# Performance work log

Hardware: AMD Instinct MI355X
Metric: run time of the kernel (lower is better)

The kernel has to match this reference:

```python
import jax, jax.numpy as jnp
import numpy as np

N_NODES = 100000
N_EDGES = 3200000
F_IN = 256
H = 256
L = 256
BN_EPS = 1e-5


def gcn_conv(x, src, dst, deg_inv_sqrt, W, b):
    # x: [N, Fin]; src/dst: [E+N] (self-loops appended); returns [N, Fout]
    h = x @ W  # dense transform first (Fout may be < Fin)
    norm = deg_inv_sqrt[src] * deg_inv_sqrt[dst]  # [E+N]
    msg = h[src] * norm[:, None]                  # gather
    out = jax.ops.segment_sum(msg, dst, num_segments=N_NODES)  # scatter-add
    return out + b


def batch_norm(x, gamma, beta):
    # BatchNorm1d in training mode: per-feature mean/var over the node dim
    mean = jnp.mean(x, axis=0)
    var = jnp.var(x, axis=0)
    return (x - mean) * jax.lax.rsqrt(var + BN_EPS) * gamma + beta


def setup_inputs() -> dict:
    key = jax.random.key(0)
    ks = jax.random.split(key, 8)
    x = jax.random.normal(ks[0], (N_NODES, F_IN), dtype=jnp.float32)
    edge_index = jax.random.randint(ks[1], (2, N_EDGES), 0, N_NODES, dtype=jnp.int64)
    # glorot-ish init for weights
    W1 = jax.random.normal(ks[2], (F_IN, H), dtype=jnp.float32) * (1.0 / np.sqrt(F_IN))
    b1 = jnp.zeros((H,), dtype=jnp.float32)
    W_mu = jax.random.normal(ks[3], (H, L), dtype=jnp.float32) * (1.0 / np.sqrt(H))
    b_mu = jnp.zeros((L,), dtype=jnp.float32)
    W_ls = jax.random.normal(ks[4], (H, L), dtype=jnp.float32) * (1.0 / np.sqrt(H))
    b_ls = jnp.zeros((L,), dtype=jnp.float32)
    gamma = jnp.ones((H,), dtype=jnp.float32)
    beta = jnp.zeros((H,), dtype=jnp.float32)
    return {"x": x, "edge_index": edge_index, "W1": W1, "b1": b1,
            "W_mu": W_mu, "b_mu": b_mu, "W_ls": W_ls, "b_ls": b_ls,
            "gamma": gamma, "beta": beta}


def reference(x, edge_index, W1, b1, W_mu, b_mu, W_ls, b_ls, gamma, beta):
    # Add self-loops once (shared across the three GCNConv layers)
    loop = jnp.arange(N_NODES, dtype=edge_index.dtype)
    src = jnp.concatenate([edge_index[0], loop])
    dst = jnp.concatenate([edge_index[1], loop])
    deg = jax.ops.segment_sum(jnp.ones_like(dst, dtype=jnp.float32), dst,
                              num_segments=N_NODES)
    deg_inv_sqrt = jnp.where(deg > 0, jax.lax.rsqrt(jnp.maximum(deg, 1.0)), 0.0)

    h = gcn_conv(x, src, dst, deg_inv_sqrt, W1, b1)
    h = jax.nn.relu(batch_norm(h, gamma, beta))
    mu = gcn_conv(h, src, dst, deg_inv_sqrt, W_mu, b_mu)
    logstd = gcn_conv(h, src, dst, deg_inv_sqrt, W_ls, b_ls)
    return (mu, logstd)
```

## Files before the change

### kernel.cpp

```cpp
#include <hip/hip_runtime.h>
#include <hip/hip_bf16.h>

#define FEAT 256
#define NPB 512
#define NPB_SHIFT 9
#define MAXBINS 256
#define CAP 20480
#define BIN_CHUNK 8192

typedef __attribute__((ext_vector_type(8))) short bf16x8;
typedef __attribute__((ext_vector_type(8))) ushort u16x8;
typedef __attribute__((ext_vector_type(4))) float f32x4;

__device__ __forceinline__ float bf2f(ushort h) {
    union { unsigned u; float f; } v; v.u = ((unsigned)h) << 16; return v.f;
}
__device__ __forceinline__ ushort f2bf(float f) {
    union { float f; unsigned u; } v; v.f = f;
    unsigned u = v.u;
    return (ushort)((u + 0x7FFFu + ((u >> 16) & 1u)) >> 16);
}


__global__ __launch_bounds__(256) void k_bin(const int* __restrict__ ei, int E, int N,
                                             int* __restrict__ bincur,
                                             int2* __restrict__ binbuf, int nbins) {
    __shared__ int hist[MAXBINS];
    __shared__ int base[MAXBINS];
    int t = threadIdx.x;
    int T = E + N;
    int start = blockIdx.x * BIN_CHUNK;
    int end = min(start + BIN_CHUNK, T);
    for (int b = t; b < nbins; b += 256) hist[b] = 0;
    __syncthreads();
    for (int idx = start + t; idx < end; idx += 256) {
        int d = (idx < E) ? ei[E + idx] : idx - E;
        atomicAdd(&hist[d >> NPB_SHIFT], 1);
    }
    __syncthreads();
    for (int b = t; b < nbins; b += 256) {
        int c = hist[b];
        base[b] = c ? (b * CAP + atomicAdd(&bincur[b], c)) : 0;
        hist[b] = 0;
    }
    __syncthreads();
    for (int idx = start + t; idx < end; idx += 256) {
        int s, d;
        if (idx < E) { s = ei[idx]; d = ei[E + idx]; }
        else         { s = idx - E; d = idx - E; }
        int b = d >> NPB_SHIFT;
        int local = atomicAdd(&hist[b], 1);
        binbuf[base[b] + local] = make_int2(s, d);
    }
}


__global__ __launch_bounds__(512) void k_scanb(const int* __restrict__ bsum,
                                               int* __restrict__ bpre,
                                               int* __restrict__ offs_n, int nb) {
    __shared__ int s[512];
    int t = threadIdx.x;
    int v = (t < nb) ? bsum[t] : 0;
    s[t] = v;
    __syncthreads();
    for (int d = 1; d < 512; d <<= 1) {
        int x = (t >= d) ? s[t - d] : 0;
        __syncthreads();
        s[t] += x;
        __syncthreads();
    }
    if (t < nb) bpre[t] = s[t] - v;
    if (t == nb - 1) offs_n[0] = s[t];
}


__global__ __launch_bounds__(512) void k_histoffs(const int2* __restrict__ binbuf,
                                                  const int* __restrict__ bincur,
                                                  const int* __restrict__ bpre,
                                                  int* __restrict__ offs,
                                                  float* __restrict__ dis, int N) {
    __shared__ int h[NPB];
    int b = blockIdx.x;
    int t = threadIdx.x;
    int node0 = b * NPB;
    int nn = min(NPB, N - node0);
    h[t] = 0;
    __syncthreads();
    int cnt = bincur[b];
    int base = b * CAP;
    for (int i = t; i < cnt; i += 512) {
        int d = binbuf[base + i].y;
        atomicAdd(&h[d - node0], 1);
    }
    __syncthreads();
    int v = h[t];
    for (int d = 1; d < 512; d <<= 1) {
        int x = (t >= d) ? h[t - d] : 0;
        __syncthreads();
        h[t] += x;
        __syncthreads();
    }
    if (t < nn) {
        offs[node0 + t] = bpre[b] + h[t] - v;
        dis[node0 + t] = rsqrtf((float)v);
    }
}


__global__ __launch_bounds__(256) void k_csr(const int2* __restrict__ binbuf,
                                             const int* __restrict__ bincur,
                                             const int* __restrict__ offs,
                                             int* __restrict__ csr, int N) {
    __shared__ int soffs[NPB + 1];
    __shared__ int cur[NPB];
    int b = blockIdx.x;
    int node0 = b * NPB;
    int nn = min(NPB, N - node0);
    int t = threadIdx.x;
    for (int i = t; i <= nn; i += 256) soffs[i] = offs[node0 + i];
    for (int i = t; i < nn; i += 256) cur[i] = 0;
    __syncthreads();
    int cnt = bincur[b];
    int base = b * CAP;
    for (int idx = t; idx < cnt; idx += 256) {
        int2 e = binbuf[base + idx];
        int ld = e.y - node0;
        int c = atomicAdd(&cur[ld], 1);
        csr[soffs[ld] + c] = e.x;
    }
}


__global__ __launch_bounds__(256) void k_cvt(const float* __restrict__ x,
                                             ushort* __restrict__ y,
                                             const float* __restrict__ dis, int n4) {
    int i = blockIdx.x * blockDim.x + threadIdx.x;
    int stride = gridDim.x * blockDim.x;
    for (; i < n4; i += stride) {
        float d = dis[i >> 6];
        float4 v = ((const float4*)x)[i];
        ushort4 o;
        o.x = f2bf(v.x * d); o.y = f2bf(v.y * d);
        o.z = f2bf(v.z * d); o.w = f2bf(v.w * d);
        ((ushort4*)y)[i] = o;
    }
}


__global__ void k_wprep(const float* __restrict__ W1, const float* __restrict__ Wmu,
                        const float* __restrict__ Wls, const float* __restrict__ bmu,
                        const float* __restrict__ bls,
                        ushort* __restrict__ Wt1, ushort* __restrict__ Wtc,
                        float* __restrict__ biasc, float* __restrict__ bnacc) {
    int i = blockIdx.x * 256 + threadIdx.x;
    int m = i >> 16;
    int j = i & 65535;
    int n = j >> 8, k = j & 255;
    const float* W = (m == 0) ? W1 : (m == 1) ? Wmu : Wls;
    ushort v = f2bf(W[k * 256 + n]);
    if (m == 0) Wt1[j] = v;
    else if (m == 1) Wtc[j] = v;
    else Wtc[65536 + j] = v;
    if (i < 512) { biasc[i] = (i < 256) ? bmu[i] : bls[i - 256]; bnacc[i] = 0.f; }
}


template <int NCOL, bool BF16OUT>
__global__ __launch_bounds__(256, 4) void k_aggmm(const ushort* __restrict__ tab,
                                                  const int* __restrict__ offs,
                                                  const int* __restrict__ csr,
                                                  const float* __restrict__ dis,
                                                  const ushort* __restrict__ Bt,
                                                  const float* __restrict__ bias,
                                                  float* __restrict__ C0,
                                                  float* __restrict__ C1,
                                                  ushort* __restrict__ Cb,
                                                  float* __restrict__ bnacc,
                                                  int N) {
    __shared__ ushort At[64 * 256];
    __shared__ ushort Bs[64 * 64];
    int t = threadIdx.x;
    int wave = t >> 6;
    int lane = t & 63;
    int half = lane >> 5;
    int l32 = lane & 31;
    int rowbase = blockIdx.x * 64;

    for (int i = 0; i < 16; ++i) {
        int r = wave * 16 + i;
        int node = rowbase + r;
        float acc[8] = {};
        if (node < N) {
            int beg = offs[node], end = offs[node + 1];
            int k = beg;
            for (; k + 16 <= end; k += 16) {
                int s0 = csr[k + half];
                int s1 = csr[k + 2 + half];
                int s2 = csr[k + 4 + half];
                int s3 = csr[k + 6 + half];
                int s4 = csr[k + 8 + half];
                int s5 = csr[k + 10 + half];
                int s6 = csr[k + 12 + half];
                int s7 = csr[k + 14 + half];
                bf16x8 v0 = *(const bf16x8*)(tab + (size_t)s0 * FEAT + l32 * 8);
                bf16x8 v1 = *(const bf16x8*)(tab + (size_t)s1 * FEAT + l32 * 8);
                bf16x8 v2 = *(const bf16x8*)(tab + (size_t)s2 * FEAT + l32 * 8);
                bf16x8 v3 = *(const bf16x8*)(tab + (size_t)s3 * FEAT + l32 * 8);
                bf16x8 v4 = *(const bf16x8*)(tab + (size_t)s4 * FEAT + l32 * 8);
                bf16x8 v5 = *(const bf16x8*)(tab + (size_t)s5 * FEAT + l32 * 8);
                bf16x8 v6 = *(const bf16x8*)(tab + (size_t)s6 * FEAT + l32 * 8);
                bf16x8 v7 = *(const bf16x8*)(tab + (size_t)s7 * FEAT + l32 * 8);
                #pragma unroll
                for (int j = 0; j < 8; ++j) {
                    float t0 = bf2f((ushort)v0[j]) + bf2f((ushort)v1[j]);
                    float t1 = bf2f((ushort)v2[j]) + bf2f((ushort)v3[j]);
                    float t2 = bf2f((ushort)v4[j]) + bf2f((ushort)v5[j]);
                    float t3 = bf2f((ushort)v6[j]) + bf2f((ushort)v7[j]);
                    acc[j] += (t0 + t1) + (t2 + t3);
                }
            }
            for (; k + 2 <= end; k += 2) {
                int s = csr[k + half];
                bf16x8 v = *(const bf16x8*)(tab + (size_t)s * FEAT + l32 * 8);
                #pragma unroll
                for (int j = 0; j < 8; ++j) acc[j] += bf2f((ushort)v[j]);
            }
            if (k < end && half == 0) {
                int s = csr[k];
                bf16x8 v = *(const bf16x8*)(tab + (size_t)s * FEAT + l32 * 8);
                #pragma unroll
                for (int j = 0; j < 8; ++j) acc[j] += bf2f((ushort)v[j]);
            }
        }
        #pragma unroll
        for (int j = 0; j < 8; ++j) acc[j] += __shfl_xor(acc[j], 32, 64);
        if (half == 0) {
            float d = (node < N) ? dis[node] : 0.f;
            u16x8 o;
            #pragma unroll
            for (int j = 0; j < 8; ++j) o[j] = f2bf(acc[j] * d);
            int cs = (l32 & 24) | ((l32 & 7) ^ (r & 7));
            *(u16x8*)(At + r * 256 + cs * 8) = o;
        }
    }
    __syncthreads();

    constexpr int NH = NCOL / 64;
    int wm = wave >> 1, wn = wave & 1;
    int lo = lane & 15, g = lane >> 4;
    for (int nh = 0; nh < NH; ++nh) {
        f32x4 acc2[2][2] = {};
        for (int kt = 0; kt < 4; ++kt) {
            #pragma unroll
            for (int u = 0; u < 2; ++u) {
                int id = t + u * 256;
                int br = id >> 3, bc = id & 7;
                int lc = bc ^ (br & 7);
                bf16x8 bv = *(const bf16x8*)(Bt + (size_t)(nh * 64 + br) * 256 + kt * 64 + lc * 8);
                *(bf16x8*)(Bs + br * 64 + bc * 8) = bv;
            }
            __syncthreads();
            #pragma unroll
            for (int h = 0; h < 2; ++h) {
                bf16x8 af[2], bfr[2];
                #pragma unroll
                for (int m = 0; m < 2; ++m) {
                    int r = wm * 32 + m * 16 + lo;
                    af[m] = *(const bf16x8*)(At + r * 256 + (kt * 8 + ((h * 4 + g) ^ (r & 7))) * 8);
                }
                #pragma unroll
                for (int n = 0; n < 2; ++n) {
                    int rb = wn * 32 + n * 16 + lo;
                    bfr[n] = *(const bf16x8*)(Bs + rb * 64 + ((h * 4 + g) ^ (rb & 7)) * 8);
                }
                #pragma unroll
                for (int m = 0; m < 2; ++m)
                    #pragma unroll
                    for (int n = 0; n < 2; ++n)
                        acc2[m][n] = __builtin_amdgcn_mfma_f32_16x16x32_bf16(
                            af[m], bfr[n], acc2[m][n], 0, 0, 0);
            }
            __syncthreads();
        }
        #pragma unroll
        for (int n = 0; n < 2; ++n) {
            int gc = nh * 64 + wn * 32 + n * 16 + lo;
            float bb = bias[gc];
            float s = 0.f, q = 0.f;
            #pragma unroll
            for (int m = 0; m < 2; ++m) {
                f32x4 v = acc2[m][n];
                #pragma unroll
                for (int r4 = 0; r4 < 4; ++r4) {
                    int grow = rowbase + wm * 32 + m * 16 + g * 4 + r4;
                    if (grow < N) {
                        float val = v[r4] + bb;
                        if (BF16OUT) {
                            Cb[(size_t)grow * 256 + gc] = f2bf(val);
                            s += val; q += val * val;
                        } else {
                            float* Cp = C0; int cc = gc;
                            if (gc >= 256) { Cp = C1; cc = gc - 256; }
                            __builtin_nontemporal_store(val, &Cp[(size_t)grow * 256 + cc]);
                        }
                    }
                }
            }
            if (BF16OUT) {
                s += __shfl_xor(s, 16, 64); s += __shfl_xor(s, 32, 64);
                q += __shfl_xor(q, 16, 64); q += __shfl_xor(q, 32, 64);
                if (g == 0) {
                    atomicAdd(&bnacc[gc], s);
                    atomicAdd(&bnacc[256 + gc], q);
                }
            }
        }
    }
}


__global__ __launch_bounds__(256) void k_bnapply(const ushort* __restrict__ h,
                                                 ushort* __restrict__ o,
                                                 const float* __restrict__ acc,
                                                 const float* __restrict__ gamma,
                                                 const float* __restrict__ beta,
                                                 const float* __restrict__ dis, int Nn) {
    int c4 = (threadIdx.x & 63) * 4;
    int rof = (int)threadIdx.x >> 6;
    float inv = 1.0f / (float)Nn;
    float g[4], b[4];
    #pragma unroll
    for (int j = 0; j < 4; ++j) {
        float mean = acc[c4 + j] * inv;
        float var = acc[FEAT + c4 + j] * inv - mean * mean;
        float rs = rsqrtf(var + 1e-5f);
        g[j] = gamma[c4 + j] * rs;
        b[j] = beta[c4 + j] - mean * g[j];
    }
    for (int r = blockIdx.x * 4 + rof; r < Nn; r += gridDim.x * 4) {
        float d = dis[r];
        ushort4 v = *(const ushort4*)(h + (size_t)r * FEAT + c4);
        float o0 = bf2f(v.x) * g[0] + b[0], o1 = bf2f(v.y) * g[1] + b[1];
        float o2 = bf2f(v.z) * g[2] + b[2], o3 = bf2f(v.w) * g[3] + b[3];
        ushort4 ov;
        ov.x = f2bf((o0 > 0.f ? o0 : 0.f) * d);
        ov.y = f2bf((o1 > 0.f ? o1 : 0.f) * d);
        ov.z = f2bf((o2 > 0.f ? o2 : 0.f) * d);
        ov.w = f2bf((o3 > 0.f ? o3 : 0.f) * d);
        *(ushort4*)(o + (size_t)r * FEAT + c4) = ov;
    }
}


extern "C" void kernel_launch(void* const* d_in, const int* in_sizes, int n_in,
                              void* d_out, int out_size, void* d_ws, size_t ws_size,
                              hipStream_t stream) {
    const float* x     = (const float*)d_in[0];
    const int*   ei    = (const int*)d_in[1];
    const float* W1    = (const float*)d_in[2];
    const float* b1    = (const float*)d_in[3];
    const float* Wmu   = (const float*)d_in[4];
    const float* bmu   = (const float*)d_in[5];
    const float* Wls   = (const float*)d_in[6];
    const float* bls   = (const float*)d_in[7];
    const float* gamma = (const float*)d_in[8];
    const float* beta  = (const float*)d_in[9];

    int N = in_sizes[0] / FEAT;
    int E = in_sizes[1] / 2;
    int nbins = (N + NPB - 1) / NPB;
    int T = E + N;

    float* out = (float*)d_out;
    float* mu  = out;
    float* ls  = out + (size_t)N * FEAT;
    ushort* xtab = (ushort*)mu;
    ushort* H1b  = (ushort*)ls;

    char* p = (char*)d_ws;
    auto alloc = [&](size_t bytes) -> void* {
        void* r = (void*)p;
        p += (bytes + 255) & ~(size_t)255;
        return r;
    };
    ushort* htab  = (ushort*)alloc((size_t)N * FEAT * 2);
    int2*   binbuf= (int2*)  alloc((size_t)nbins * CAP * 8);
    int*    csr   = (int*)   alloc((size_t)T * 4);
    int*    offs  = (int*)   alloc((size_t)(N + 1) * 4);
    float*  dis   = (float*) alloc((size_t)N * 4);
    float*  bnacc = (float*) alloc(512 * 4);
    ushort* Wt1   = (ushort*)alloc(65536 * 2);
    ushort* Wtc   = (ushort*)alloc(131072 * 2);
    float*  biasc = (float*) alloc(512 * 4);
    int*    bpre  = (int*)   alloc((size_t)nbins * 4);
    int*    bincur= (int*)   alloc((size_t)nbins * 4);

    hipMemsetAsync(bincur, 0, (size_t)nbins * 4, stream);
    k_bin<<<(T + BIN_CHUNK - 1) / BIN_CHUNK, 256, 0, stream>>>(ei, E, N, bincur, binbuf, nbins);

    k_scanb<<<1, 512, 0, stream>>>(bincur, bpre, offs + N, nbins);
    k_histoffs<<<nbins, 512, 0, stream>>>(binbuf, bincur, bpre, offs, dis, N);
    k_csr<<<nbins, 256, 0, stream>>>(binbuf, bincur, offs, csr, N);

    k_wprep<<<768, 256, 0, stream>>>(W1, Wmu, Wls, bmu, bls, Wt1, Wtc, biasc, bnacc);
    k_cvt<<<2048, 256, 0, stream>>>(x, xtab, dis, N * FEAT / 4);

    int gblocks = (N + 63) / 64;

    k_aggmm<256, true><<<gblocks, 256, 0, stream>>>(
        xtab, offs, csr, dis, Wt1, b1, nullptr, nullptr, H1b, bnacc, N);

    k_bnapply<<<2048, 256, 0, stream>>>(H1b, htab, bnacc, gamma, beta, dis, N);

    k_aggmm<512, false><<<gblocks, 256, 0, stream>>>(
        htab, offs, csr, dis, Wtc, biasc, mu, ls, nullptr, nullptr, N);
}
```

Baseline: 791.9 us.

## Fuse histogram and CSR fill kernels; load B fragments directly from global

```diff
diff --git a/kernel.cpp b/kernel.cpp
--- a/kernel.cpp
+++ b/kernel.cpp
@@ -74,23 +74,24 @@
 }
 
 
-__global__ __launch_bounds__(512) void k_histoffs(const int2* __restrict__ binbuf,
-                                                  const int* __restrict__ bincur,
-                                                  const int* __restrict__ bpre,
-                                                  int* __restrict__ offs,
-                                                  float* __restrict__ dis, int N) {
+__global__ __launch_bounds__(512) void k_histcsr(const int2* __restrict__ binbuf,
+                                                 const int* __restrict__ bincur,
+                                                 const int* __restrict__ bpre,
+                                                 int* __restrict__ offs,
+                                                 float* __restrict__ dis,
+                                                 int* __restrict__ csr, int N) {
     __shared__ int h[NPB];
+    __shared__ int cur[NPB];
     int b = blockIdx.x;
     int t = threadIdx.x;
     int node0 = b * NPB;
     int nn = min(NPB, N - node0);
-    h[t] = 0;
+    h[t] = 0; cur[t] = 0;
     __syncthreads();
     int cnt = bincur[b];
     int base = b * CAP;
     for (int i = t; i < cnt; i += 512) {
-        int d = binbuf[base + i].y;
-        atomicAdd(&h[d - node0], 1);
+        atomicAdd(&h[binbuf[base + i].y - node0], 1);
     }
     __syncthreads();
     int v = h[t];
@@ -100,33 +101,18 @@
         h[t] += x;
         __syncthreads();
     }
+    int myoff = bpre[b] + h[t] - v;
     if (t < nn) {
-        offs[node0 + t] = bpre[b] + h[t] - v;
+        offs[node0 + t] = myoff;
         dis[node0 + t] = rsqrtf((float)v);
     }
-}
-
-
-__global__ __launch_bounds__(256) void k_csr(const int2* __restrict__ binbuf,
-                                             const int* __restrict__ bincur,
-                                             const int* __restrict__ offs,
-                                             int* __restrict__ csr, int N) {
-    __shared__ int soffs[NPB + 1];
-    __shared__ int cur[NPB];
-    int b = blockIdx.x;
-    int node0 = b * NPB;
-    int nn = min(NPB, N - node0);
-    int t = threadIdx.x;
-    for (int i = t; i <= nn; i += 256) soffs[i] = offs[node0 + i];
-    for (int i = t; i < nn; i += 256) cur[i] = 0;
-    __syncthreads();
-    int cnt = bincur[b];
-    int base = b * CAP;
-    for (int idx = t; idx < cnt; idx += 256) {
-        int2 e = binbuf[base + idx];
+    h[t] = myoff;
+    __syncthreads();
+    for (int i = t; i < cnt; i += 512) {
+        int2 e = binbuf[base + i];
         int ld = e.y - node0;
         int c = atomicAdd(&cur[ld], 1);
-        csr[soffs[ld] + c] = e.x;
+        csr[h[ld] + c] = e.x;
     }
 }
 
@@ -166,7 +152,7 @@
 
 
 template <int NCOL, bool BF16OUT>
-__global__ __launch_bounds__(256, 4) void k_aggmm(const ushort* __restrict__ tab,
+__global__ __launch_bounds__(256, 5) void k_aggmm(const ushort* __restrict__ tab,
                                                   const int* __restrict__ offs,
                                                   const int* __restrict__ csr,
                                                   const float* __restrict__ dis,
@@ -178,7 +164,6 @@
                                                   float* __restrict__ bnacc,
                                                   int N) {
     __shared__ ushort At[64 * 256];
-    __shared__ ushort Bs[64 * 64];
     int t = threadIdx.x;
     int wave = t >> 6;
     int lane = t & 63;
@@ -250,16 +235,8 @@
     int lo = lane & 15, g = lane >> 4;
     for (int nh = 0; nh < NH; ++nh) {
         f32x4 acc2[2][2] = {};
+        #pragma unroll
         for (int kt = 0; kt < 4; ++kt) {
-            #pragma unroll
-            for (int u = 0; u < 2; ++u) {
-                int id = t + u * 256;
-                int br = id >> 3, bc = id & 7;
-                int lc = bc ^ (br & 7);
-                bf16x8 bv = *(const bf16x8*)(Bt + (size_t)(nh * 64 + br) * 256 + kt * 64 + lc * 8);
-                *(bf16x8*)(Bs + br * 64 + bc * 8) = bv;
-            }
-            __syncthreads();
             #pragma unroll
             for (int h = 0; h < 2; ++h) {
                 bf16x8 af[2], bfr[2];
@@ -270,8 +247,8 @@
                 }
                 #pragma unroll
                 for (int n = 0; n < 2; ++n) {
-                    int rb = wn * 32 + n * 16 + lo;
-                    bfr[n] = *(const bf16x8*)(Bs + rb * 64 + ((h * 4 + g) ^ (rb & 7)) * 8);
+                    int rb = nh * 64 + wn * 32 + n * 16 + lo;
+                    bfr[n] = *(const bf16x8*)(Bt + (size_t)rb * 256 + kt * 64 + (h * 4 + g) * 8);
                 }
                 #pragma unroll
                 for (int m = 0; m < 2; ++m)
@@ -280,7 +257,6 @@
                         acc2[m][n] = __builtin_amdgcn_mfma_f32_16x16x32_bf16(
                             af[m], bfr[n], acc2[m][n], 0, 0, 0);
             }
-            __syncthreads();
         }
         #pragma unroll
         for (int n = 0; n < 2; ++n) {
@@ -399,8 +375,7 @@
     k_bin<<<(T + BIN_CHUNK - 1) / BIN_CHUNK, 256, 0, stream>>>(ei, E, N, bincur, binbuf, nbins);
 
     k_scanb<<<1, 512, 0, stream>>>(bincur, bpre, offs + N, nbins);
-    k_histoffs<<<nbins, 512, 0, stream>>>(binbuf, bincur, bpre, offs, dis, N);
-    k_csr<<<nbins, 256, 0, stream>>>(binbuf, bincur, offs, csr, N);
+    k_histcsr<<<nbins, 512, 0, stream>>>(binbuf, bincur, bpre, offs, dis, csr, N);
 
     k_wprep<<<768, 256, 0, stream>>>(W1, Wmu, Wls, bmu, bls, Wt1, Wtc, biasc, bnacc);
     k_cvt<<<2048, 256, 0, stream>>>(x, xtab, dis, N * FEAT / 4);
```

Measured after the change: 914.4 us. +15.5%, slower.
